# Optimization experiments

Hardware: AMD Instinct MI355X
Metric: run time of the kernel (lower is better)

Reference implementation:

```python
import jax, jax.numpy as jnp
import numpy as np
import math

N, D, H, E, ED = 2048, 256, 8, 65536, 64
HD = D // H  # head_dim = 32


def _layernorm(x, g, b, eps=1e-5):
    mu = jnp.mean(x, axis=-1, keepdims=True)
    var = jnp.mean((x - mu) ** 2, axis=-1, keepdims=True)
    return (x - mu) * jax.lax.rsqrt(var + eps) * g + b


def setup_inputs() -> dict:
    key = jax.random.key(0)
    ks = jax.random.split(key, 24)
    s = 0.02
    inp = {
        "x": jax.random.normal(ks[0], (N, D), jnp.float32),
        "edge_index": jax.random.randint(ks[1], (2, E), 0, N, jnp.int64),
        "edge_attr": jax.random.normal(ks[2], (E, ED), jnp.float32),
        # attention projections (stored [in, out]; y = x @ W + b)
        "Wq": jax.random.normal(ks[3], (D, D), jnp.float32) * s,
        "bq": jnp.zeros((D,), jnp.float32),
        "Wk": jax.random.normal(ks[4], (D, D), jnp.float32) * s,
        "bk": jnp.zeros((D,), jnp.float32),
        "Wv": jax.random.normal(ks[5], (D, D), jnp.float32) * s,
        "bv": jnp.zeros((D,), jnp.float32),
        "Wo": jax.random.normal(ks[6], (D, D), jnp.float32) * s,
        "bo": jnp.zeros((D,), jnp.float32),
        # edge bias projection: edge_dim -> num_heads
        "We": jax.random.normal(ks[7], (ED, H), jnp.float32) * s,
        "be": jnp.zeros((H,), jnp.float32),
        # FFN
        "W1": jax.random.normal(ks[8], (D, 4 * D), jnp.float32) * s,
        "b1": jnp.zeros((4 * D,), jnp.float32),
        "W2": jax.random.normal(ks[9], (4 * D, D), jnp.float32) * s,
        "b2": jnp.zeros((D,), jnp.float32),
        # layernorms
        "ln1_g": jnp.ones((D,), jnp.float32),
        "ln1_b": jnp.zeros((D,), jnp.float32),
        "ln2_g": jnp.ones((D,), jnp.float32),
        "ln2_b": jnp.zeros((D,), jnp.float32),
    }
    return inp


def reference(x, edge_index, edge_attr, Wq, bq, Wk, bk, Wv, bv, Wo, bo,
              We, be, W1, b1, W2, b2, ln1_g, ln1_b, ln2_g, ln2_b):
    n = x.shape[0]
    scale = math.sqrt(HD)
    src, dst = edge_index[0], edge_index[1]

    residual = x
    h = _layernorm(x, ln1_g, ln1_b)
    Q = (h @ Wq + bq).reshape(n, H, HD)
    K = (h @ Wk + bk).reshape(n, H, HD)
    V = (h @ Wv + bv).reshape(n, H, HD)

    # dense [N, N, H] scores, matching the original einsum
    scores = jnp.einsum('nhd,mhd->nmh', Q, K) / scale

    # adjacency mask with self-loops (scatter .set semantics, like torch assignment)
    diag = jnp.arange(n)
    adj = jnp.zeros((n, n), jnp.bool_).at[src, dst].set(True)
    adj = adj.at[diag, diag].set(True)

    # edge bias scattered into [N, N, H] (assignment semantics)
    edge_bias = edge_attr @ We + be  # [E, H]
    bias = jnp.zeros((n, n, H), scores.dtype).at[src, dst].set(edge_bias)
    scores = scores + bias

    scores = jnp.where(adj[:, :, None], scores, -jnp.inf)
    # softmax over dim=1 (source/key nodes m)
    attn = jax.nn.softmax(scores, axis=1)

    out = jnp.einsum('nmh,mhd->nhd', attn, V).reshape(n, D)
    out = out @ Wo + bo
    x = residual + out

    residual = x
    h2 = _layernorm(x, ln2_g, ln2_b)
    ffn = jax.nn.gelu(h2 @ W1 + b1, approximate=False) @ W2 + b2
    return residual + ffn
```

## Files before the change

### kernel.cpp

```cpp
#include <hip/hip_runtime.h>
#include <math.h>

#define D 256
#define NH 8
#define HD 32
#define EDIM 64
#define MAXDEG 192

typedef __attribute__((ext_vector_type(8))) short bfrag;
typedef __attribute__((ext_vector_type(4))) float ffrag;

__device__ __forceinline__ unsigned short f2bf(float x) {
  unsigned int u = __float_as_uint(x);
  return (unsigned short)((u + 0x7FFFu + ((u >> 16) & 1u)) >> 16);
}

__global__ __launch_bounds__(256) void prep_kernel(
    const float* __restrict__ s0, const float* __restrict__ s1,
    const float* __restrict__ s2, const float* __restrict__ s3,
    const float* __restrict__ s4, const float* __restrict__ s5,
    unsigned short* __restrict__ d0, unsigned short* __restrict__ d1,
    unsigned short* __restrict__ d2, unsigned short* __restrict__ d3,
    unsigned short* __restrict__ d4, unsigned short* __restrict__ d5,
    const float* __restrict__ x, const float* __restrict__ g,
    const float* __restrict__ b, unsigned short* __restrict__ hbf,
    const int* __restrict__ ei, int* __restrict__ cnt,
    int* __restrict__ colp, int* __restrict__ eidxp,
    const float* __restrict__ ea, const float* __restrict__ We,
    const float* __restrict__ be, float* __restrict__ eb,
    int N, int E, int CB, int EB) {
  int blk = blockIdx.x;
  int tid = threadIdx.x;
  if (blk < CB) {
    int i = (blk * 256 + tid) * 4;
    const float* s; unsigned short* d; int off;
    if      (i < 65536)  { s = s0; d = d0; off = i; }
    else if (i < 131072) { s = s1; d = d1; off = i - 65536; }
    else if (i < 196608) { s = s2; d = d2; off = i - 131072; }
    else if (i < 262144) { s = s3; d = d3; off = i - 196608; }
    else if (i < 524288) { s = s4; d = d4; off = i - 262144; }
    else if (i < 786432) { s = s5; d = d5; off = i - 524288; }
    else return;
    float4 v = *(const float4*)(s + off);
    *(ushort4*)(d + off) = make_ushort4(f2bf(v.x), f2bf(v.y), f2bf(v.z), f2bf(v.w));
  } else if (blk < CB + N) {
    int row = blk - CB;
    float v = x[row * D + tid];
    float s = v, sq = v * v;
    #pragma unroll
    for (int m = 1; m < 64; m <<= 1) { s += __shfl_xor(s, m); sq += __shfl_xor(sq, m); }
    __shared__ float ps[4], pq[4];
    int wid = tid >> 6, lane = tid & 63;
    if (lane == 0) { ps[wid] = s; pq[wid] = sq; }
    __syncthreads();
    float ts = ps[0] + ps[1] + ps[2] + ps[3];
    float tq = pq[0] + pq[1] + pq[2] + pq[3];
    float mu  = ts * (1.f / D);
    float var = tq * (1.f / D) - mu * mu;
    float inv = 1.f / sqrtf(var + 1e-5f);
    hbf[row * D + tid] = f2bf((v - mu) * inv * g[tid] + b[tid]);
  } else if (blk < CB + N + EB) {
    int e = (blk - CB - N) * 256 + tid;
    if (e >= E) return;
    const float* row = ea + (size_t)e * EDIM;
    float acc[NH];
    #pragma unroll
    for (int h = 0; h < NH; h++) acc[h] = be[h];
    #pragma unroll 4
    for (int k = 0; k < EDIM; k++) {
      float r = row[k];
      #pragma unroll
      for (int h = 0; h < NH; h++) acc[h] = fmaf(r, We[k * NH + h], acc[h]);
    }
    #pragma unroll
    for (int h = 0; h < NH; h++) eb[e * NH + h] = acc[h];
  } else {
    int e = (blk - CB - N - EB) * 256 + tid;
    if (e >= E) return;
    int s = ei[e], d = ei[E + e];
    int pos = atomicAdd(&cnt[s], 1);
    if (pos < MAXDEG) {
      colp [(size_t)s * MAXDEG + pos] = d;
      eidxp[(size_t)s * MAXDEG + pos] = e;
    }
  }
}

__device__ __forceinline__ void mg_core(const unsigned short* __restrict__ A,
    const unsigned short* __restrict__ B, int K, int Nn, int bm, int bn,
    int kb0, int kb1, unsigned short (*As)[40], unsigned short (*Bt)[40],
    ffrag acc[4]) {
  int tid = threadIdx.x;
  int wid = tid >> 6, lane = tid & 63;
  int lr = lane & 15, lk = lane >> 4;
  int ar = tid >> 2, ak = (tid & 3) * 8;
  int bnn = tid & 63, bkg = tid >> 6;
  for (int kb = kb0; kb < kb1; kb += 32) {
    uint4 av = *(const uint4*)(A + (size_t)(bm + ar) * K + kb + ak);
    *(uint4*)&As[ar][ak] = av;
    unsigned int u[4];
    #pragma unroll
    for (int jj = 0; jj < 4; jj++) {
      unsigned short lo = B[(size_t)(kb + bkg * 8 + 2 * jj)     * Nn + bn + bnn];
      unsigned short hi = B[(size_t)(kb + bkg * 8 + 2 * jj + 1) * Nn + bn + bnn];
      u[jj] = (unsigned int)lo | ((unsigned int)hi << 16);
    }
    *(uint4*)&Bt[bnn][bkg * 8] = make_uint4(u[0], u[1], u[2], u[3]);
    __syncthreads();
    bfrag af = *(const bfrag*)&As[wid * 16 + lr][lk * 8];
    #pragma unroll
    for (int nf = 0; nf < 4; nf++) {
      bfrag bf = *(const bfrag*)&Bt[nf * 16 + lr][lk * 8];
      acc[nf] = __builtin_amdgcn_mfma_f32_16x16x32_bf16(af, bf, acc[nf], 0, 0, 0);
    }
    __syncthreads();
  }
}

__global__ __launch_bounds__(256) void mgemm_qkv(const unsigned short* __restrict__ A,
    const unsigned short* __restrict__ B0, const unsigned short* __restrict__ B1,
    const unsigned short* __restrict__ B2,
    const float* __restrict__ b0, const float* __restrict__ b1, const float* __restrict__ b2,
    float* __restrict__ C0, float* __restrict__ C1, float* __restrict__ C2,
    int M, int Nn, int K) {
  __shared__ __align__(16) unsigned short As[64][40];
  __shared__ __align__(16) unsigned short Bt[64][40];
  int z = blockIdx.z;
  const unsigned short* B = (z == 0) ? B0 : (z == 1) ? B1 : B2;
  const float* bias = (z == 0) ? b0 : (z == 1) ? b1 : b2;
  float* C = (z == 0) ? C0 : (z == 1) ? C1 : C2;
  int bm = blockIdx.y * 64, bn = blockIdx.x * 64;
  ffrag acc[4] = {};
  mg_core(A, B, K, Nn, bm, bn, 0, K, As, Bt, acc);
  int lane = threadIdx.x & 63, wid = threadIdx.x >> 6;
  int lr = lane & 15, lk = lane >> 4;
  #pragma unroll
  for (int nf = 0; nf < 4; nf++) {
    int col = bn + nf * 16 + lr;
    float bv = bias[col];
    #pragma unroll
    for (int i = 0; i < 4; i++) {
      int row = bm + wid * 16 + lk * 4 + i;
      C[(size_t)row * Nn + col] = acc[nf][i] + bv;
    }
  }
}

__global__ __launch_bounds__(256) void mgemm_res(const unsigned short* __restrict__ A,
    const unsigned short* __restrict__ B, const float* __restrict__ bias,
    const float* __restrict__ R, float* __restrict__ C, int M, int Nn, int K) {
  __shared__ __align__(16) unsigned short As[64][40];
  __shared__ __align__(16) unsigned short Bt[64][40];
  int bm = blockIdx.y * 64, bn = blockIdx.x * 64;
  ffrag acc[4] = {};
  mg_core(A, B, K, Nn, bm, bn, 0, K, As, Bt, acc);
  int lane = threadIdx.x & 63, wid = threadIdx.x >> 6;
  int lr = lane & 15, lk = lane >> 4;
  #pragma unroll
  for (int nf = 0; nf < 4; nf++) {
    int col = bn + nf * 16 + lr;
    float bv = bias[col];
    #pragma unroll
    for (int i = 0; i < 4; i++) {
      int row = bm + wid * 16 + lk * 4 + i;
      C[(size_t)row * Nn + col] = acc[nf][i] + bv + R[(size_t)row * Nn + col];
    }
  }
}

__global__ __launch_bounds__(256) void mgemm_gelu(const unsigned short* __restrict__ A,
    const unsigned short* __restrict__ B, const float* __restrict__ bias,
    unsigned short* __restrict__ C, int M, int Nn, int K) {
  __shared__ __align__(16) unsigned short As[64][40];
  __shared__ __align__(16) unsigned short Bt[64][40];
  int bm = blockIdx.y * 64, bn = blockIdx.x * 64;
  ffrag acc[4] = {};
  mg_core(A, B, K, Nn, bm, bn, 0, K, As, Bt, acc);
  int lane = threadIdx.x & 63, wid = threadIdx.x >> 6;
  int lr = lane & 15, lk = lane >> 4;
  #pragma unroll
  for (int nf = 0; nf < 4; nf++) {
    int col = bn + nf * 16 + lr;
    float bv = bias[col];
    #pragma unroll
    for (int i = 0; i < 4; i++) {
      int row = bm + wid * 16 + lk * 4 + i;
      float v = acc[nf][i] + bv;
      v = 0.5f * v * (1.f + erff(v * 0.70710678118654752f));
      C[(size_t)row * Nn + col] = f2bf(v);
    }
  }
}

__global__ __launch_bounds__(256) void ln2_kernel(const float* __restrict__ x,
    const float* __restrict__ g, const float* __restrict__ b,
    unsigned short* __restrict__ out) {
  int row = blockIdx.x;
  int tid = threadIdx.x;
  float v = x[row * D + tid];
  float s = v, sq = v * v;
  #pragma unroll
  for (int m = 1; m < 64; m <<= 1) { s += __shfl_xor(s, m); sq += __shfl_xor(sq, m); }
  __shared__ float ps[4], pq[4];
  int wid = tid >> 6, lane = tid & 63;
  if (lane == 0) { ps[wid] = s; pq[wid] = sq; }
  __syncthreads();
  float ts = ps[0] + ps[1] + ps[2] + ps[3];
  float tq = pq[0] + pq[1] + pq[2] + pq[3];
  float mu  = ts * (1.f / D);
  float var = tq * (1.f / D) - mu * mu;
  float inv = 1.f / sqrtf(var + 1e-5f);
  out[row * D + tid] = f2bf((v - mu) * inv * g[tid] + b[tid]);
}

__global__ __launch_bounds__(256) void attn_kernel(const float* __restrict__ Q,
    const float* __restrict__ Km, const float* __restrict__ Vm,
    const float* __restrict__ eb, const int* __restrict__ cnt,
    const int* __restrict__ colp, const int* __restrict__ eidxp,
    unsigned short* __restrict__ out, int N) {
  int wid = threadIdx.x >> 6, lane = threadIdx.x & 63;
  int n = blockIdx.x * 4 + wid;
  if (n >= N) return;
  int h = lane >> 3, j = lane & 7;
  int off = h * HD + j * 4;
  float4 q = *(const float4*)(Q + (size_t)n * D + off);
  int L = cnt[n];
  if (L > MAXDEG) L = MAXDEG;
  size_t base = (size_t)n * MAXDEG;
  int dv0 = -1, dv1 = -1, dv2 = -1;
  int ev0 = -1, ev1 = -1, ev2 = -1;
  if (lane       < L) { dv0 = colp[base + lane      ]; ev0 = eidxp[base + lane      ]; }
  if (lane +  64 < L) { dv1 = colp[base + lane +  64]; ev1 = eidxp[base + lane +  64]; }
  if (lane + 128 < L) { dv2 = colp[base + lane + 128]; ev2 = eidxp[base + lane + 128]; }
  bool self_present = __any(dv0 == n) || __any(dv1 == n) || __any(dv2 == n);
  float mrun = -INFINITY, srun = 0.f;
  float4 acc = make_float4(0.f, 0.f, 0.f, 0.f);

#define PROC_EDGE(m_, bias_) {                                                 \
    float4 k4 = *(const float4*)(Km + (size_t)(m_) * D + off);                 \
    float dot = q.x * k4.x + q.y * k4.y + q.z * k4.z + q.w * k4.w;             \
    dot += __shfl_xor(dot, 1); dot += __shfl_xor(dot, 2); dot += __shfl_xor(dot, 4); \
    float sc = fmaf(dot, 0.17677669529663687f, bias_);                         \
    float mnew = fmaxf(mrun, sc);                                              \
    float corr = __expf(mrun - mnew);                                          \
    float pp = __expf(sc - mnew);                                              \
    float4 v4 = *(const float4*)(Vm + (size_t)(m_) * D + off);                 \
    srun = srun * corr + pp;                                                   \
    acc.x = fmaf(acc.x, corr, pp * v4.x);                                      \
    acc.y = fmaf(acc.y, corr, pp * v4.y);                                      \
    acc.z = fmaf(acc.z, corr, pp * v4.z);                                      \
    acc.w = fmaf(acc.w, corr, pp * v4.w);                                      \
    mrun = mnew; }

#define PROC_CHUNK(dvC, evC, base_) {                                          \
    int cl = L - (base_); if (cl > 64) cl = 64;                                \
    for (int ii = 0; ii < cl; ii++) {                                          \
      int d_i = __shfl(dvC, ii);                                               \
      int e_i = __shfl(evC, ii);                                               \
      bool dom = (dv0 == d_i && ev0 > e_i) || (dv1 == d_i && ev1 > e_i) ||     \
                 (dv2 == d_i && ev2 > e_i);                                    \
      if (__any(dom)) continue;                                                \
      float bias_ = eb[(size_t)e_i * NH + h];                                  \
      PROC_EDGE(d_i, bias_);                                                   \
    } }

  PROC_CHUNK(dv0, ev0, 0)
  if (L > 64)  PROC_CHUNK(dv1, ev1, 64)
  if (L > 128) PROC_CHUNK(dv2, ev2, 128)
  if (!self_present) PROC_EDGE(n, 0.f)
#undef PROC_CHUNK
#undef PROC_EDGE

  float inv = 1.f / srun;
  ushort4 o = make_ushort4(f2bf(acc.x * inv), f2bf(acc.y * inv),
                           f2bf(acc.z * inv), f2bf(acc.w * inv));
  *(ushort4*)(out + (size_t)n * D + off) = o;
}

extern "C" void kernel_launch(void* const* d_in, const int* in_sizes, int n_in,
                              void* d_out, int out_size, void* d_ws, size_t ws_size,
                              hipStream_t stream) {
  const float* x    = (const float*)d_in[0];
  const int*   ei   = (const int*)d_in[1];
  const float* ea   = (const float*)d_in[2];
  const float* Wq   = (const float*)d_in[3];  const float* bq = (const float*)d_in[4];
  const float* Wk   = (const float*)d_in[5];  const float* bk = (const float*)d_in[6];
  const float* Wv   = (const float*)d_in[7];  const float* bv = (const float*)d_in[8];
  const float* Wo   = (const float*)d_in[9];  const float* bo = (const float*)d_in[10];
  const float* We   = (const float*)d_in[11]; const float* be = (const float*)d_in[12];
  const float* W1   = (const float*)d_in[13]; const float* b1 = (const float*)d_in[14];
  const float* W2   = (const float*)d_in[15]; const float* b2 = (const float*)d_in[16];
  const float* ln1g = (const float*)d_in[17]; const float* ln1b = (const float*)d_in[18];
  const float* ln2g = (const float*)d_in[19]; const float* ln2b = (const float*)d_in[20];

  int N = in_sizes[0] / D;
  int E = in_sizes[1] / 2;

  char* p = (char*)d_ws;
  auto alloc = [&](size_t bytes) -> char* {
    char* r = p; p += (bytes + 255) & ~(size_t)255; return r;
  };
  unsigned short* hbf    = (unsigned short*)alloc((size_t)N * D * 2);
  float*          Qd     = (float*)         alloc((size_t)N * D * 4);
  float*          Kd     = (float*)         alloc((size_t)N * D * 4);
  float*          Vd     = (float*)         alloc((size_t)N * D * 4);
  unsigned short* attnbf = (unsigned short*)alloc((size_t)N * D * 2);
  float*          x_mid  = (float*)         alloc((size_t)N * D * 4);
  float*          ebuf   = (float*)         alloc((size_t)E * NH * 4);
  unsigned short* tbf    = (unsigned short*)alloc((size_t)N * 4 * D * 2);
  unsigned short* Wqb    = (unsigned short*)alloc((size_t)D * D * 2);
  unsigned short* Wkb    = (unsigned short*)alloc((size_t)D * D * 2);
  unsigned short* Wvb    = (unsigned short*)alloc((size_t)D * D * 2);
  unsigned short* Wob    = (unsigned short*)alloc((size_t)D * D * 2);
  unsigned short* W1b    = (unsigned short*)alloc((size_t)D * 4 * D * 2);
  unsigned short* W2b    = (unsigned short*)alloc((size_t)4 * D * D * 2);
  int*            cnt    = (int*)           alloc((size_t)N * 4);
  int*            colp   = (int*)           alloc((size_t)N * MAXDEG * 4);
  int*            eidxp  = (int*)           alloc((size_t)N * MAXDEG * 4);

  hipMemsetAsync(cnt, 0, (size_t)N * 4, stream);

  int CB = 768;
  int EB = (E + 255) / 256;

  prep_kernel<<<CB + N + 2 * EB, 256, 0, stream>>>(
      Wq, Wk, Wv, Wo, W1, W2, Wqb, Wkb, Wvb, Wob, W1b, W2b,
      x, ln1g, ln1b, hbf, ei, cnt, colp, eidxp, ea, We, be, ebuf, N, E, CB, EB);
  dim3 g_qkv(D / 64, N / 64, 3);
  mgemm_qkv<<<g_qkv, 256, 0, stream>>>(hbf, Wqb, Wkb, Wvb, bq, bk, bv,
                                       Qd, Kd, Vd, N, D, D);
  attn_kernel<<<(N + 3) / 4, 256, 0, stream>>>(Qd, Kd, Vd, ebuf, cnt, colp, eidxp,
                                               attnbf, N);
  dim3 g_o(D / 64, N / 64);
  mgemm_res<<<g_o, 256, 0, stream>>>(attnbf, Wob, bo, x, x_mid, N, D, D);
  ln2_kernel<<<N, 256, 0, stream>>>(x_mid, ln2g, ln2b, hbf);
  dim3 g_1(4 * D / 64, N / 64);
  mgemm_gelu<<<g_1, 256, 0, stream>>>(hbf, W1b, b1, tbf, N, 4 * D, D);
  mgemm_res<<<g_o, 256, 0, stream>>>(tbf, W2b, b2, x_mid, (float*)d_out, N, D, 4 * D);
}
```

Before: 197.6 us.

## Split-K the output and FFN2 GEMMs with fused partial-sum reduction

Both N×D-output GEMMs launched only 128 blocks, which underfills the GPU. They now use split-K (2 slices for Wo, 4 for W2) and write partial sums to a workspace. For Wo, the reduction, bias and residual are folded into the LN2 kernel. For W2, a separate vectorised reduce kernel adds the bias and residual. This buys more parallelism at the cost of extra partial-buffer traffic and, for W2, one more launch.

```diff
diff --git a/kernel.cpp b/kernel.cpp
--- a/kernel.cpp
+++ b/kernel.cpp
@@ -146,24 +146,25 @@
   }
 }
 
-__global__ __launch_bounds__(256) void mgemm_res(const unsigned short* __restrict__ A,
-    const unsigned short* __restrict__ B, const float* __restrict__ bias,
-    const float* __restrict__ R, float* __restrict__ C, int M, int Nn, int K) {
+__global__ __launch_bounds__(256) void mgemm_splitk(const unsigned short* __restrict__ A,
+    const unsigned short* __restrict__ B, float* __restrict__ P,
+    int M, int Nn, int K, int Kslice) {
   __shared__ __align__(16) unsigned short As[64][40];
   __shared__ __align__(16) unsigned short Bt[64][40];
+  int z = blockIdx.z;
   int bm = blockIdx.y * 64, bn = blockIdx.x * 64;
   ffrag acc[4] = {};
-  mg_core(A, B, K, Nn, bm, bn, 0, K, As, Bt, acc);
+  mg_core(A, B, K, Nn, bm, bn, z * Kslice, (z + 1) * Kslice, As, Bt, acc);
+  float* Pz = P + (size_t)z * M * Nn;
   int lane = threadIdx.x & 63, wid = threadIdx.x >> 6;
   int lr = lane & 15, lk = lane >> 4;
   #pragma unroll
   for (int nf = 0; nf < 4; nf++) {
     int col = bn + nf * 16 + lr;
-    float bv = bias[col];
     #pragma unroll
     for (int i = 0; i < 4; i++) {
       int row = bm + wid * 16 + lk * 4 + i;
-      C[(size_t)row * Nn + col] = acc[nf][i] + bv + R[(size_t)row * Nn + col];
+      Pz[(size_t)row * Nn + col] = acc[nf][i];
     }
   }
 }
@@ -192,12 +193,32 @@
   }
 }
 
-__global__ __launch_bounds__(256) void ln2_kernel(const float* __restrict__ x,
+__global__ __launch_bounds__(256) void reduce_kernel(const float* __restrict__ P,
+    const float* __restrict__ bias, const float* __restrict__ R,
+    float* __restrict__ out, int MN, int Nn, int S) {
+  int i = blockIdx.x * 256 + threadIdx.x;
+  if (i * 4 >= MN) return;
+  size_t b = (size_t)i * 4;
+  float4 acc = *(const float4*)(P + b);
+  for (int s = 1; s < S; s++) {
+    float4 p = *(const float4*)(P + (size_t)s * MN + b);
+    acc.x += p.x; acc.y += p.y; acc.z += p.z; acc.w += p.w;
+  }
+  float4 bi = *(const float4*)(bias + (b % Nn));
+  float4 r  = *(const float4*)(R + b);
+  acc.x += bi.x + r.x; acc.y += bi.y + r.y; acc.z += bi.z + r.z; acc.w += bi.w + r.w;
+  *(float4*)(out + b) = acc;
+}
+
+__global__ __launch_bounds__(256) void ln2_fused_kernel(const float* __restrict__ P,
+    const float* __restrict__ bo, const float* __restrict__ x,
     const float* __restrict__ g, const float* __restrict__ b,
-    unsigned short* __restrict__ out) {
+    float* __restrict__ x_mid, unsigned short* __restrict__ hbf, int MN) {
   int row = blockIdx.x;
   int tid = threadIdx.x;
-  float v = x[row * D + tid];
+  size_t idx = (size_t)row * D + tid;
+  float v = P[idx] + P[(size_t)MN + idx] + bo[tid] + x[idx];
+  x_mid[idx] = v;
   float s = v, sq = v * v;
   #pragma unroll
   for (int m = 1; m < 64; m <<= 1) { s += __shfl_xor(s, m); sq += __shfl_xor(sq, m); }
@@ -210,7 +231,7 @@
   float mu  = ts * (1.f / D);
   float var = tq * (1.f / D) - mu * mu;
   float inv = 1.f / sqrtf(var + 1e-5f);
-  out[row * D + tid] = f2bf((v - mu) * inv * g[tid] + b[tid]);
+  hbf[idx] = f2bf((v - mu) * inv * g[tid] + b[tid]);
 }
 
 __global__ __launch_bounds__(256) void attn_kernel(const float* __restrict__ Q,
@@ -308,6 +329,7 @@
   float*          x_mid  = (float*)         alloc((size_t)N * D * 4);
   float*          ebuf   = (float*)         alloc((size_t)E * NH * 4);
   unsigned short* tbf    = (unsigned short*)alloc((size_t)N * 4 * D * 2);
+  float*          P      = (float*)         alloc((size_t)4 * N * D * 4);
   unsigned short* Wqb    = (unsigned short*)alloc((size_t)D * D * 2);
   unsigned short* Wkb    = (unsigned short*)alloc((size_t)D * D * 2);
   unsigned short* Wvb    = (unsigned short*)alloc((size_t)D * D * 2);
@@ -320,6 +342,7 @@
 
   hipMemsetAsync(cnt, 0, (size_t)N * 4, stream);
 
+  int MN = N * D;
   int CB = 768;
   int EB = (E + 255) / 256;
 
@@ -331,10 +354,17 @@
                                        Qd, Kd, Vd, N, D, D);
   attn_kernel<<<(N + 3) / 4, 256, 0, stream>>>(Qd, Kd, Vd, ebuf, cnt, colp, eidxp,
                                                attnbf, N);
-  dim3 g_o(D / 64, N / 64);
-  mgemm_res<<<g_o, 256, 0, stream>>>(attnbf, Wob, bo, x, x_mid, N, D, D);
-  ln2_kernel<<<N, 256, 0, stream>>>(x_mid, ln2g, ln2b, hbf);
+  {
+    dim3 g(D / 64, N / 64, 2);
+    mgemm_splitk<<<g, 256, 0, stream>>>(attnbf, Wob, P, N, D, D, D / 2);
+    ln2_fused_kernel<<<N, 256, 0, stream>>>(P, bo, x, ln2g, ln2b, x_mid, hbf, MN);
+  }
   dim3 g_1(4 * D / 64, N / 64);
   mgemm_gelu<<<g_1, 256, 0, stream>>>(hbf, W1b, b1, tbf, N, 4 * D, D);
-  mgemm_res<<<g_o, 256, 0, stream>>>(tbf, W2b, b2, x_mid, (float*)d_out, N, D, 4 * D);
-}
+  {
+    dim3 g(D / 64, N / 64, 4);
+    mgemm_splitk<<<g, 256, 0, stream>>>(tbf, W2b, P, N, D, 4 * D, D);
+    reduce_kernel<<<(MN / 4 + 255) / 256, 256, 0, stream>>>(P, b2, x_mid, (float*)d_out,
+                                                            MN, D, 4);
+  }
+}
```

Result: faster. 187.3 us (-5.2%).
